# Performance work log

Hardware: AMD Instinct MI355X
Metric: run time of the kernel (lower is better)

Reference implementation:

```python
import jax, jax.numpy as jnp
import numpy as np

FEAT_SIZE, HIDDEN_SIZE, ATT_SIZE = 2048, 1024, 512
BATCH, FEAT_NUM = 64, 512


def setup_inputs() -> dict:
    key = jax.random.key(0)
    ks = jax.random.split(key, 8)
    s = lambda fan_in: 1.0 / np.sqrt(fan_in)
    return {
        "feats": jax.random.normal(ks[0], (BATCH, FEAT_NUM, FEAT_SIZE), jnp.float32),
        "key": jax.random.normal(ks[1], (BATCH, HIDDEN_SIZE), jnp.float32),
        "wh_w": jax.random.uniform(ks[2], (ATT_SIZE, HIDDEN_SIZE), jnp.float32, -s(HIDDEN_SIZE), s(HIDDEN_SIZE)),
        "wh_b": jax.random.uniform(ks[3], (ATT_SIZE,), jnp.float32, -s(HIDDEN_SIZE), s(HIDDEN_SIZE)),
        "wv_w": jax.random.uniform(ks[4], (ATT_SIZE, FEAT_SIZE), jnp.float32, -s(FEAT_SIZE), s(FEAT_SIZE)),
        "wv_b": jax.random.uniform(ks[5], (ATT_SIZE,), jnp.float32, -s(FEAT_SIZE), s(FEAT_SIZE)),
        "wa_w": jax.random.uniform(ks[6], (1, ATT_SIZE), jnp.float32, -s(ATT_SIZE), s(ATT_SIZE)),
    }


def reference(feats, key, wh_w, wh_b, wv_w, wv_b, wa_w):
    # v = wv(feats): (B, N, A)
    v = jnp.einsum('bnf,af->bna', feats, wv_w) + wv_b
    # h = wh(key): (B, A), broadcast-added over feat_num
    h = key @ wh_w.T + wh_b
    inputs = h[:, None, :] + v                       # (B, N, A)
    scores = jnp.einsum('bna,a->bn', jnp.tanh(inputs), wa_w[0])  # (B, N)
    alpha = jax.nn.softmax(scores, axis=1)           # (B, N)
    att_feats = jnp.einsum('bn,bnf->bf', alpha, feats)  # (B, F)
    return (att_feats, alpha)
```

## Files before the change

kernel.cpp:

```cpp
#include <hip/hip_runtime.h>
#include <hip/hip_bf16.h>

#define FEATSZ 2048
#define HIDSZ  1024
#define ATTSZ  512
#define BATCH  64
#define FEATN  512

typedef float  f32x4  __attribute__((ext_vector_type(4)));
typedef __bf16 bf16x8 __attribute__((ext_vector_type(8)));

__device__ __forceinline__ unsigned short f2bf(float f) {
    union { float f; unsigned int u; } x; x.f = f;
    unsigned int u = x.u;
    return (unsigned short)((u + 0x7fffu + ((u >> 16) & 1u)) >> 16);
}

__global__ void k_h(const float* __restrict__ key, const float* __restrict__ wh_w,
                    const float* __restrict__ wh_b, float* __restrict__ h) {
    const int b = blockIdx.y;
    const int ac = blockIdx.x;
    const int t = threadIdx.x;
    const int lane = t & 63, wv = t >> 6;
    float k16[16];
    const float* kb = key + b * HIDSZ;
#pragma unroll
    for (int j = 0; j < 16; ++j) k16[j] = kb[lane + 64 * j];
#pragma unroll 1
    for (int i = 0; i < 16; ++i) {
        int a = ac * 64 + wv * 16 + i;
        const float* wr = wh_w + (size_t)a * HIDSZ;
        float s = 0.f;
#pragma unroll
        for (int j = 0; j < 16; ++j) s += k16[j] * wr[lane + 64 * j];
#pragma unroll
        for (int d = 32; d; d >>= 1) s += __shfl_xor(s, d);
        if (lane == 0) h[b * ATTSZ + a] = s + wh_b[a];
    }
}

__global__ void k_wvcvt(const float* __restrict__ wv_w, unsigned short* __restrict__ wvb) {
    int idx = blockIdx.x * 256 + threadIdx.x;
    int a = idx >> 11, k = idx & 2047;
    int CF = a >> 4, c = a & 15, ks = k >> 5, kin = k & 31;
    int lane = c + ((kin >> 3) << 4);
    int dst = ((ks * 32 + CF) * 64 + lane) * 8 + (kin & 7);
    wvb[dst] = f2bf(wv_w[idx]);
}

__global__ __launch_bounds__(512) void k_scores(
        const float* __restrict__ feats, const unsigned short* __restrict__ wvb,
        const float* __restrict__ h, const float* __restrict__ wv_b,
        const float* __restrict__ wa, float* __restrict__ scores) {
    __shared__ __align__(16) unsigned long long Alds[2][512];
    __shared__ float hb[ATTSZ];
    __shared__ float wal[ATTSZ];
    __shared__ float scp[8][64];

    const int t = threadIdx.x;
    const int lane = t & 63, w = t >> 6;
    const int m0 = blockIdx.x * 64;
    const int b = m0 >> 9;

    hb[t]  = h[b * ATTSZ + t] + wv_b[t];
    wal[t] = wa[t];

    const int row = t >> 3, kq = t & 7;
    const float* gp = feats + (size_t)(m0 + row) * FEATSZ + kq * 4;

    auto stA = [&](int buf, float4 v) {
        unsigned long long u = (unsigned long long)f2bf(v.x)
                             | ((unsigned long long)f2bf(v.y) << 16)
                             | ((unsigned long long)f2bf(v.z) << 32)
                             | ((unsigned long long)f2bf(v.w) << 48);
        int idx8 = (row * 8 + kq) ^ ((row & 7) << 1);
        Alds[buf][idx8] = u;
    };

    float4 a0 = *(const float4*)gp;
    stA(0, a0);

    const unsigned short* wb = wvb + w * 2048 + lane * 8;
    bf16x8 bcur[4];
#pragma unroll
    for (int cf = 0; cf < 4; ++cf) bcur[cf] = *(const bf16x8*)(wb + cf * 512);

    const char* abase = (const char*)&Alds[0][0];
    int raddr[4];
#pragma unroll
    for (int m = 0; m < 4; ++m) {
        int r = m * 16 + (lane & 15);
        raddr[m] = ((r * 64) + ((lane >> 4) * 16)) ^ ((r & 7) << 4);
    }

    f32x4 acc[4][4];
#pragma unroll
    for (int m = 0; m < 4; ++m)
#pragma unroll
        for (int cf = 0; cf < 4; ++cf) acc[m][cf] = (f32x4)0.0f;

    __syncthreads();

    int cur = 0;
#pragma unroll 2
    for (int it = 0; it < 64; ++it) {
        float4 anxt;
        bf16x8 bnxt[4];
        if (it < 63) {
            anxt = *(const float4*)(gp + (it + 1) * 32);
            const unsigned short* wbn = wb + (it + 1) * 16384;
#pragma unroll
            for (int cf = 0; cf < 4; ++cf) bnxt[cf] = *(const bf16x8*)(wbn + cf * 512);
        }
        bf16x8 af[4];
#pragma unroll
        for (int m = 0; m < 4; ++m)
            af[m] = *(const bf16x8*)__builtin_assume_aligned(abase + cur * 4096 + raddr[m], 16);
#pragma unroll
        for (int m = 0; m < 4; ++m)
#pragma unroll
            for (int cf = 0; cf < 4; ++cf)
                acc[m][cf] = __builtin_amdgcn_mfma_f32_16x16x32_bf16(af[m], bcur[cf], acc[m][cf], 0, 0, 0);
        if (it < 63) stA(cur ^ 1, anxt);
        __syncthreads();
        if (it < 63) {
#pragma unroll
            for (int cf = 0; cf < 4; ++cf) bcur[cf] = bnxt[cf];
        }
        cur ^= 1;
    }

    float p[4][4];
#pragma unroll
    for (int m = 0; m < 4; ++m)
#pragma unroll
        for (int j = 0; j < 4; ++j) p[m][j] = 0.f;

    const int c = lane & 15, q = lane >> 4;
#pragma unroll
    for (int m = 0; m < 4; ++m)
#pragma unroll
        for (int cf = 0; cf < 4; ++cf) {
            int a = w * 64 + cf * 16 + c;
            float hba = hb[a], waa = wal[a];
#pragma unroll
            for (int j = 0; j < 4; ++j)
                p[m][j] += tanhf(acc[m][cf][j] + hba) * waa;
        }
#pragma unroll
    for (int m = 0; m < 4; ++m)
#pragma unroll
        for (int j = 0; j < 4; ++j) {
            float v = p[m][j];
            v += __shfl_xor(v, 1); v += __shfl_xor(v, 2);
            v += __shfl_xor(v, 4); v += __shfl_xor(v, 8);
            p[m][j] = v;
        }
    if (c == 0) {
#pragma unroll
        for (int m = 0; m < 4; ++m)
#pragma unroll
            for (int j = 0; j < 4; ++j)
                scp[w][m * 16 + q * 4 + j] = p[m][j];
    }
    __syncthreads();
    if (t < 64) {
        float s = 0.f;
#pragma unroll
        for (int ww = 0; ww < 8; ++ww) s += scp[ww][t];
        scores[m0 + t] = s;
    }
}

__global__ void k_softmax(const float* __restrict__ scores, float* __restrict__ alpha) {
    __shared__ float red[16];
    const int b = blockIdx.x, t = threadIdx.x;
    const int lane = t & 63, w = t >> 6;
    float s = scores[b * FEATN + t];
    float m = s;
#pragma unroll
    for (int d = 32; d; d >>= 1) m = fmaxf(m, __shfl_xor(m, d));
    if (lane == 0) red[w] = m;
    __syncthreads();
    if (t == 0) {
        float mm = red[0];
        for (int i = 1; i < 8; ++i) mm = fmaxf(mm, red[i]);
        red[8] = mm;
    }
    __syncthreads();
    float e = __expf(s - red[8]);
    float sum = e;
#pragma unroll
    for (int d = 32; d; d >>= 1) sum += __shfl_xor(sum, d);
    if (lane == 0) red[w] = sum;
    __syncthreads();
    if (t == 0) {
        float ss = 0.f;
        for (int i = 0; i < 8; ++i) ss += red[i];
        red[9] = 1.0f / ss;
    }
    __syncthreads();
    alpha[b * FEATN + t] = e * red[9];
}

__global__ void k_att_part(const float* __restrict__ feats, const float* __restrict__ alpha,
                           float* __restrict__ part) {
    const int b = blockIdx.x, fc = blockIdx.y, ns = blockIdx.z, t = threadIdx.x;
    const int f0 = fc * 1024 + t * 4;
    const float* fp = feats + (size_t)(b * FEATN + ns * 128) * FEATSZ + f0;
    const float* al = alpha + b * FEATN + ns * 128;
    float4 acc = {0.f, 0.f, 0.f, 0.f};
#pragma unroll 4
    for (int i = 0; i < 128; ++i) {
        float a = al[i];
        float4 v = *(const float4*)(fp + (size_t)i * FEATSZ);
        acc.x += a * v.x; acc.y += a * v.y; acc.z += a * v.z; acc.w += a * v.w;
    }
    *(float4*)(part + ((size_t)ns * BATCH + b) * FEATSZ + f0) = acc;
}

__global__ void k_att_red(const float* __restrict__ part, float* __restrict__ out) {
    const int idx = (blockIdx.x * 256 + threadIdx.x) * 4;
    float4 s = *(const float4*)(part + idx);
#pragma unroll
    for (int z = 1; z < 4; ++z) {
        float4 v = *(const float4*)(part + (size_t)z * (BATCH * FEATSZ) + idx);
        s.x += v.x; s.y += v.y; s.z += v.z; s.w += v.w;
    }
    *(float4*)(out + idx) = s;
}

extern "C" void kernel_launch(void* const* d_in, const int* in_sizes, int n_in,
                              void* d_out, int out_size, void* d_ws, size_t ws_size,
                              hipStream_t stream) {
    const float* feats = (const float*)d_in[0];
    const float* key   = (const float*)d_in[1];
    const float* wh_w  = (const float*)d_in[2];
    const float* wh_b  = (const float*)d_in[3];
    const float* wv_w  = (const float*)d_in[4];
    const float* wv_b  = (const float*)d_in[5];
    const float* wa_w  = (const float*)d_in[6];

    float* out_att   = (float*)d_out;
    float* out_alpha = out_att + BATCH * FEATSZ;

    char* ws = (char*)d_ws;
    float* h              = (float*)(ws);
    float* scores         = (float*)(ws + 131072);
    unsigned short* wvb   = (unsigned short*)(ws + 262144);
    float* part           = (float*)(ws + 262144);

    hipLaunchKernelGGL(k_h,        dim3(8, 64),    dim3(256), 0, stream, key, wh_w, wh_b, h);
    hipLaunchKernelGGL(k_wvcvt,    dim3(4096),     dim3(256), 0, stream, wv_w, wvb);
    hipLaunchKernelGGL(k_scores,   dim3(512),      dim3(512), 0, stream, feats, wvb, h, wv_b, wa_w, scores);
    hipLaunchKernelGGL(k_softmax,  dim3(64),       dim3(512), 0, stream, scores, out_alpha);
    hipLaunchKernelGGL(k_att_part, dim3(64, 2, 4), dim3(256), 0, stream, feats, out_alpha, part);
    hipLaunchKernelGGL(k_att_red,  dim3(128),      dim3(256), 0, stream, part, out_att);
}
```

Before: 190.6 us.

## Stream fp32 feats directly into LDS with global_load_lds and larger K stages

Replaces the register-staged load, bf16 convert and LDS store of the feats tile with asynchronous global_load_lds transfers of raw fp32 into a swizzled, double-buffered 64 KB LDS region. Each stage now covers 128 K elements, so there are far fewer barriers, and the bf16 packing moves to the consumer side with v_cvt_pk_bf16_f32 after the LDS read. The hb/wal LDS staging is replaced by per-lane register loads in the epilogue. The trade-off is double the LDS traffic and footprint per tile, which limits how many blocks fit per CU, and it relies on the compiler waiting on the async loads before each barrier.

```diff
diff --git a/kernel.cpp b/kernel.cpp
--- a/kernel.cpp
+++ b/kernel.cpp
@@ -48,50 +48,46 @@
     wvb[dst] = f2bf(wv_w[idx]);
 }
 
-__global__ __launch_bounds__(512) void k_scores(
+__global__ __launch_bounds__(512, 4) void k_scores(
         const float* __restrict__ feats, const unsigned short* __restrict__ wvb,
         const float* __restrict__ h, const float* __restrict__ wv_b,
         const float* __restrict__ wa, float* __restrict__ scores) {
-    __shared__ __align__(16) unsigned long long Alds[2][512];
-    __shared__ float hb[ATTSZ];
-    __shared__ float wal[ATTSZ];
-    __shared__ float scp[8][64];
-
+    __shared__ __align__(16) char smem[65536];
     const int t = threadIdx.x;
     const int lane = t & 63, w = t >> 6;
     const int m0 = blockIdx.x * 64;
     const int b = m0 >> 9;
 
-    hb[t]  = h[b * ATTSZ + t] + wv_b[t];
-    wal[t] = wa[t];
-
-    const int row = t >> 3, kq = t & 7;
-    const float* gp = feats + (size_t)(m0 + row) * FEATSZ + kq * 4;
-
-    auto stA = [&](int buf, float4 v) {
-        unsigned long long u = (unsigned long long)f2bf(v.x)
-                             | ((unsigned long long)f2bf(v.y) << 16)
-                             | ((unsigned long long)f2bf(v.z) << 32)
-                             | ((unsigned long long)f2bf(v.w) << 48);
-        int idx8 = (row * 8 + kq) ^ ((row & 7) << 1);
-        Alds[buf][idx8] = u;
+    const char* fbase = (const char*)feats;
+    unsigned int goff[4];
+    unsigned int ldst[4];
+#pragma unroll
+    for (int s = 0; s < 4; ++s) {
+        int q = w * 256 + s * 64 + lane;
+        int r = q >> 5;
+        int c = (q & 31) ^ (r & 7);
+        goff[s] = (unsigned int)(((m0 + r) * 2048 + c * 4) * 4);
+        ldst[s] = (unsigned int)(w * 4096 + s * 1024);
+    }
+
+    const int A0 = (lane & 15) * 512 + ((((lane >> 4) * 2)    ) ^ (lane & 7)) * 16;
+    const int A1 = (lane & 15) * 512 + ((((lane >> 4) * 2) | 1) ^ (lane & 7)) * 16;
+
+    auto stage = [&](int bufc, int it) {
+#pragma unroll
+        for (int s = 0; s < 4; ++s)
+            __builtin_amdgcn_global_load_lds(
+                (const __attribute__((address_space(1))) void*)(fbase + goff[s] + it * 512),
+                (__attribute__((address_space(3))) void*)(smem + bufc * 32768 + ldst[s]),
+                16, 0, 0);
     };
 
-    float4 a0 = *(const float4*)gp;
-    stA(0, a0);
-
     const unsigned short* wb = wvb + w * 2048 + lane * 8;
-    bf16x8 bcur[4];
-#pragma unroll
-    for (int cf = 0; cf < 4; ++cf) bcur[cf] = *(const bf16x8*)(wb + cf * 512);
-
-    const char* abase = (const char*)&Alds[0][0];
-    int raddr[4];
-#pragma unroll
-    for (int m = 0; m < 4; ++m) {
-        int r = m * 16 + (lane & 15);
-        raddr[m] = ((r * 64) + ((lane >> 4) * 16)) ^ ((r & 7) << 4);
-    }
+    bf16x8 bn[4];
+    auto loadB = [&](int kk) {
+#pragma unroll
+        for (int cf = 0; cf < 4; ++cf) bn[cf] = *(const bf16x8*)(wb + kk * 16384 + cf * 512);
+    };
 
     f32x4 acc[4][4];
 #pragma unroll
@@ -99,53 +95,65 @@
 #pragma unroll
         for (int cf = 0; cf < 4; ++cf) acc[m][cf] = (f32x4)0.0f;
 
-    __syncthreads();
-
-    int cur = 0;
-#pragma unroll 2
-    for (int it = 0; it < 64; ++it) {
-        float4 anxt;
-        bf16x8 bnxt[4];
-        if (it < 63) {
-            anxt = *(const float4*)(gp + (it + 1) * 32);
-            const unsigned short* wbn = wb + (it + 1) * 16384;
-#pragma unroll
-            for (int cf = 0; cf < 4; ++cf) bnxt[cf] = *(const bf16x8*)(wbn + cf * 512);
+    stage(0, 0);
+    loadB(0);
+    __syncthreads();
+
+    auto kiter = [&](int it, int bufc) {
+        if (it < 15) stage(bufc ^ 1, it + 1);
+#pragma unroll
+        for (int ks = 0; ks < 4; ++ks) {
+            bf16x8 bc[4];
+#pragma unroll
+            for (int cf = 0; cf < 4; ++cf) bc[cf] = bn[cf];
+            int kk = it * 4 + ks + 1; if (kk > 63) kk = 63;
+            loadB(kk);
+#pragma unroll
+            for (int m = 0; m < 4; ++m) {
+                const char* ap = (const char*)smem + bufc * 32768 + m * 8192 + ks * 128;
+                f32x4 fa = *(const f32x4*)(ap + A0);
+                f32x4 fb = *(const f32x4*)(ap + A1);
+                unsigned int q0, q1, q2, q3;
+                asm("v_cvt_pk_bf16_f32 %0, %1, %2" : "=v"(q0) : "v"(fa.x), "v"(fa.y));
+                asm("v_cvt_pk_bf16_f32 %0, %1, %2" : "=v"(q1) : "v"(fa.z), "v"(fa.w));
+                asm("v_cvt_pk_bf16_f32 %0, %1, %2" : "=v"(q2) : "v"(fb.x), "v"(fb.y));
+                asm("v_cvt_pk_bf16_f32 %0, %1, %2" : "=v"(q3) : "v"(fb.z), "v"(fb.w));
+                union { unsigned int u[4]; bf16x8 v; } af;
+                af.u[0] = q0; af.u[1] = q1; af.u[2] = q2; af.u[3] = q3;
+#pragma unroll
+                for (int cf = 0; cf < 4; ++cf)
+                    acc[m][cf] = __builtin_amdgcn_mfma_f32_16x16x32_bf16(af.v, bc[cf], acc[m][cf], 0, 0, 0);
+            }
         }
-        bf16x8 af[4];
-#pragma unroll
-        for (int m = 0; m < 4; ++m)
-            af[m] = *(const bf16x8*)__builtin_assume_aligned(abase + cur * 4096 + raddr[m], 16);
-#pragma unroll
-        for (int m = 0; m < 4; ++m)
-#pragma unroll
-            for (int cf = 0; cf < 4; ++cf)
-                acc[m][cf] = __builtin_amdgcn_mfma_f32_16x16x32_bf16(af[m], bcur[cf], acc[m][cf], 0, 0, 0);
-        if (it < 63) stA(cur ^ 1, anxt);
         __syncthreads();
-        if (it < 63) {
-#pragma unroll
-            for (int cf = 0; cf < 4; ++cf) bcur[cf] = bnxt[cf];
-        }
-        cur ^= 1;
-    }
-
+    };
+
+#pragma unroll 1
+    for (int it2 = 0; it2 < 8; ++it2) {
+        kiter(it2 * 2, 0);
+        kiter(it2 * 2 + 1, 1);
+    }
+
+    const int c16 = lane & 15, q4 = lane >> 4;
+    float hreg[4], wreg[4];
+#pragma unroll
+    for (int cf = 0; cf < 4; ++cf) {
+        int a = w * 64 + cf * 16 + c16;
+        hreg[cf] = h[b * ATTSZ + a] + wv_b[a];
+        wreg[cf] = wa[a];
+    }
     float p[4][4];
 #pragma unroll
     for (int m = 0; m < 4; ++m)
 #pragma unroll
         for (int j = 0; j < 4; ++j) p[m][j] = 0.f;
-
-    const int c = lane & 15, q = lane >> 4;
 #pragma unroll
     for (int m = 0; m < 4; ++m)
 #pragma unroll
         for (int cf = 0; cf < 4; ++cf) {
-            int a = w * 64 + cf * 16 + c;
-            float hba = hb[a], waa = wal[a];
 #pragma unroll
             for (int j = 0; j < 4; ++j)
-                p[m][j] += tanhf(acc[m][cf][j] + hba) * waa;
+                p[m][j] += tanhf(acc[m][cf][j] + hreg[cf]) * wreg[cf];
         }
 #pragma unroll
     for (int m = 0; m < 4; ++m)
@@ -156,18 +164,19 @@
             v += __shfl_xor(v, 4); v += __shfl_xor(v, 8);
             p[m][j] = v;
         }
-    if (c == 0) {
+    float* scp = (float*)smem;
+    if (c16 == 0) {
 #pragma unroll
         for (int m = 0; m < 4; ++m)
 #pragma unroll
             for (int j = 0; j < 4; ++j)
-                scp[w][m * 16 + q * 4 + j] = p[m][j];
+                scp[w * 64 + m * 16 + q4 * 4 + j] = p[m][j];
     }
     __syncthreads();
     if (t < 64) {
         float s = 0.f;
 #pragma unroll
-        for (int ww = 0; ww < 8; ++ww) s += scp[ww][t];
+        for (int ww = 0; ww < 8; ++ww) s += scp[ww * 64 + t];
         scores[m0 + t] = s;
     }
 }
```

Measured after the change: 174.1 us. -8.6%, faster.

## Rewrite scores GEMM to load A directly into registers with larger tiles

Applied to the files above, without the earlier changes.

The scores kernel no longer stages the feats tile through double-buffered LDS. Each wave now loads its fp32 A fragments straight from global memory into registers, converts them to bf16 in place, and prefetches the next k-step. Each block now covers 128 rows with a 2x4 wave grid, giving 8 column fragments per wave, and the grid shrinks from 512 to 256 blocks. The per-iteration block barrier is removed, and s_setprio is placed around the MFMA bursts. The cost is higher register pressure from 32 accumulators plus prefetch buffers, under launch_bounds(512,2). Each wave also issues uncoalesced-ish strided global loads and gets no A reuse across the four column waves, so each feats row is fetched four times through cache.

```diff
diff --git a/kernel.cpp b/kernel.cpp
--- a/kernel.cpp
+++ b/kernel.cpp
@@ -48,126 +48,102 @@
     wvb[dst] = f2bf(wv_w[idx]);
 }
 
-__global__ __launch_bounds__(512) void k_scores(
+__global__ __launch_bounds__(512, 2) void k_scores(
         const float* __restrict__ feats, const unsigned short* __restrict__ wvb,
         const float* __restrict__ h, const float* __restrict__ wv_b,
         const float* __restrict__ wa, float* __restrict__ scores) {
-    __shared__ __align__(16) unsigned long long Alds[2][512];
-    __shared__ float hb[ATTSZ];
-    __shared__ float wal[ATTSZ];
-    __shared__ float scp[8][64];
-
-    const int t = threadIdx.x;
-    const int lane = t & 63, w = t >> 6;
-    const int m0 = blockIdx.x * 64;
-    const int b = m0 >> 9;
-
-    hb[t]  = h[b * ATTSZ + t] + wv_b[t];
-    wal[t] = wa[t];
-
-    const int row = t >> 3, kq = t & 7;
-    const float* gp = feats + (size_t)(m0 + row) * FEATSZ + kq * 4;
-
-    auto stA = [&](int buf, float4 v) {
-        unsigned long long u = (unsigned long long)f2bf(v.x)
-                             | ((unsigned long long)f2bf(v.y) << 16)
-                             | ((unsigned long long)f2bf(v.z) << 32)
-                             | ((unsigned long long)f2bf(v.w) << 48);
-        int idx8 = (row * 8 + kq) ^ ((row & 7) << 1);
-        Alds[buf][idx8] = u;
+    __shared__ float scp[4][128];
+    const int t = threadIdx.x, lane = t & 63, w = t >> 6;
+    const int wr = w >> 2, wc = w & 3;
+    const int m0 = blockIdx.x * 128, b = blockIdx.x >> 2;
+
+    const float* ab = feats + (size_t)(m0 + wr * 64 + (lane & 15)) * FEATSZ + (lane >> 4) * 8;
+    const unsigned short* wb = wvb + (wc * 8) * 512 + lane * 8;
+
+    f32x4 acc[4][8];
+#pragma unroll
+    for (int m = 0; m < 4; ++m)
+#pragma unroll
+        for (int cf = 0; cf < 8; ++cf) acc[m][cf] = (f32x4)0.0f;
+
+    f32x4 aA[4], aB[4];
+    bf16x8 B[2][8];
+
+    auto loadA = [&](int m, int kk, f32x4& x, f32x4& y) {
+        const float* p = ab + (size_t)m * 16 * FEATSZ + kk * 32;
+        x = *(const f32x4*)p;
+        y = *(const f32x4*)(p + 4);
     };
 
-    float4 a0 = *(const float4*)gp;
-    stA(0, a0);
-
-    const unsigned short* wb = wvb + w * 2048 + lane * 8;
-    bf16x8 bcur[4];
-#pragma unroll
-    for (int cf = 0; cf < 4; ++cf) bcur[cf] = *(const bf16x8*)(wb + cf * 512);
-
-    const char* abase = (const char*)&Alds[0][0];
-    int raddr[4];
-#pragma unroll
-    for (int m = 0; m < 4; ++m) {
-        int r = m * 16 + (lane & 15);
-        raddr[m] = ((r * 64) + ((lane >> 4) * 16)) ^ ((r & 7) << 4);
-    }
-
-    f32x4 acc[4][4];
-#pragma unroll
-    for (int m = 0; m < 4; ++m)
-#pragma unroll
-        for (int cf = 0; cf < 4; ++cf) acc[m][cf] = (f32x4)0.0f;
-
-    __syncthreads();
-
-    int cur = 0;
+#pragma unroll
+    for (int m = 0; m < 4; ++m) loadA(m, 0, aA[m], aB[m]);
+#pragma unroll
+    for (int cf = 0; cf < 8; ++cf) B[0][cf] = *(const bf16x8*)(wb + (0 * 32 + cf) * 512);
+
 #pragma unroll 2
-    for (int it = 0; it < 64; ++it) {
-        float4 anxt;
-        bf16x8 bnxt[4];
-        if (it < 63) {
-            anxt = *(const float4*)(gp + (it + 1) * 32);
-            const unsigned short* wbn = wb + (it + 1) * 16384;
-#pragma unroll
-            for (int cf = 0; cf < 4; ++cf) bnxt[cf] = *(const bf16x8*)(wbn + cf * 512);
+    for (int kk = 0; kk < 64; ++kk) {
+        const int p = kk & 1;
+        const int kn = kk < 63 ? kk + 1 : 63;
+#pragma unroll
+        for (int m = 0; m < 4; ++m) {
+            bf16x8 af;
+            af[0] = (__bf16)aA[m][0]; af[1] = (__bf16)aA[m][1];
+            af[2] = (__bf16)aA[m][2]; af[3] = (__bf16)aA[m][3];
+            af[4] = (__bf16)aB[m][0]; af[5] = (__bf16)aB[m][1];
+            af[6] = (__bf16)aB[m][2]; af[7] = (__bf16)aB[m][3];
+            loadA(m, kn, aA[m], aB[m]);
+            if (m == 0) {
+#pragma unroll
+                for (int cf = 0; cf < 8; ++cf)
+                    B[p ^ 1][cf] = *(const bf16x8*)(wb + (kn * 32 + cf) * 512);
+            }
+            __builtin_amdgcn_s_setprio(1);
+#pragma unroll
+            for (int cf = 0; cf < 8; ++cf)
+                acc[m][cf] = __builtin_amdgcn_mfma_f32_16x16x32_bf16(af, B[p][cf], acc[m][cf], 0, 0, 0);
+            __builtin_amdgcn_s_setprio(0);
         }
-        bf16x8 af[4];
-#pragma unroll
-        for (int m = 0; m < 4; ++m)
-            af[m] = *(const bf16x8*)__builtin_assume_aligned(abase + cur * 4096 + raddr[m], 16);
-#pragma unroll
-        for (int m = 0; m < 4; ++m)
-#pragma unroll
-            for (int cf = 0; cf < 4; ++cf)
-                acc[m][cf] = __builtin_amdgcn_mfma_f32_16x16x32_bf16(af[m], bcur[cf], acc[m][cf], 0, 0, 0);
-        if (it < 63) stA(cur ^ 1, anxt);
-        __syncthreads();
-        if (it < 63) {
-#pragma unroll
-            for (int cf = 0; cf < 4; ++cf) bcur[cf] = bnxt[cf];
-        }
-        cur ^= 1;
-    }
-
-    float p[4][4];
-#pragma unroll
-    for (int m = 0; m < 4; ++m)
-#pragma unroll
-        for (int j = 0; j < 4; ++j) p[m][j] = 0.f;
-
-    const int c = lane & 15, q = lane >> 4;
-#pragma unroll
-    for (int m = 0; m < 4; ++m)
-#pragma unroll
-        for (int cf = 0; cf < 4; ++cf) {
-            int a = w * 64 + cf * 16 + c;
-            float hba = hb[a], waa = wal[a];
+    }
+
+    const int c16 = lane & 15, q4 = lane >> 4;
+    float hreg[8], wreg[8];
+#pragma unroll
+    for (int cf = 0; cf < 8; ++cf) {
+        int a = wc * 128 + cf * 16 + c16;
+        hreg[cf] = h[b * ATTSZ + a] + wv_b[a];
+        wreg[cf] = wa[a];
+    }
+    float pv[4][4];
+#pragma unroll
+    for (int m = 0; m < 4; ++m)
+#pragma unroll
+        for (int j = 0; j < 4; ++j) pv[m][j] = 0.f;
+#pragma unroll
+    for (int m = 0; m < 4; ++m)
+#pragma unroll
+        for (int cf = 0; cf < 8; ++cf)
 #pragma unroll
             for (int j = 0; j < 4; ++j)
-                p[m][j] += tanhf(acc[m][cf][j] + hba) * waa;
-        }
+                pv[m][j] += tanhf(acc[m][cf][j] + hreg[cf]) * wreg[cf];
 #pragma unroll
     for (int m = 0; m < 4; ++m)
 #pragma unroll
         for (int j = 0; j < 4; ++j) {
-            float v = p[m][j];
+            float v = pv[m][j];
             v += __shfl_xor(v, 1); v += __shfl_xor(v, 2);
             v += __shfl_xor(v, 4); v += __shfl_xor(v, 8);
-            p[m][j] = v;
+            pv[m][j] = v;
         }
-    if (c == 0) {
+    if (c16 == 0) {
 #pragma unroll
         for (int m = 0; m < 4; ++m)
 #pragma unroll
             for (int j = 0; j < 4; ++j)
-                scp[w][m * 16 + q * 4 + j] = p[m][j];
-    }
-    __syncthreads();
-    if (t < 64) {
-        float s = 0.f;
-#pragma unroll
-        for (int ww = 0; ww < 8; ++ww) s += scp[ww][t];
+                scp[wc][wr * 64 + m * 16 + q4 * 4 + j] = pv[m][j];
+    }
+    __syncthreads();
+    if (t < 128) {
+        float s = scp[0][t] + scp[1][t] + scp[2][t] + scp[3][t];
         scores[m0 + t] = s;
     }
 }
@@ -252,7 +228,7 @@
 
     hipLaunchKernelGGL(k_h,        dim3(8, 64),    dim3(256), 0, stream, key, wh_w, wh_b, h);
     hipLaunchKernelGGL(k_wvcvt,    dim3(4096),     dim3(256), 0, stream, wv_w, wvb);
-    hipLaunchKernelGGL(k_scores,   dim3(512),      dim3(512), 0, stream, feats, wvb, h, wv_b, wa_w, scores);
+    hipLaunchKernelGGL(k_scores,   dim3(256),      dim3(512), 0, stream, feats, wvb, h, wv_b, wa_w, scores);
     hipLaunchKernelGGL(k_softmax,  dim3(64),       dim3(512), 0, stream, scores, out_alpha);
     hipLaunchKernelGGL(k_att_part, dim3(64, 2, 4), dim3(256), 0, stream, feats, out_alpha, part);
     hipLaunchKernelGGL(k_att_red,  dim3(128),      dim3(256), 0, stream, part, out_att);
```

After: 246.4 us. 29.3% more time.
